# Performance work log

Measured on AMD Instinct MI355X. Metric: run time of the kernel, lower is better.

Reference implementation:

```python
import jax, jax.numpy as jnp
import numpy as np

B, S, C = 4096, 6, 2048  # batch, num_strips, in_channel
D = C // 8               # query/key projection dim

def setup_inputs() -> dict:
    key = jax.random.key(0)
    k1, k2, k3, k4 = jax.random.split(key, 4)
    sc = 1.0 / np.sqrt(C)
    return {
        "x": jax.random.normal(k1, (B, S, C), dtype=jnp.float32),
        "Wq": jax.random.normal(k2, (D, C), dtype=jnp.float32) * sc,
        "Wk": jax.random.normal(k3, (D, C), dtype=jnp.float32) * sc,
        "Wv": jax.random.normal(k4, (C, C), dtype=jnp.float32) * sc,
        "gamma": jnp.ones((1,), dtype=jnp.float32),
    }

def reference(x, Wq, Wk, Wv, gamma):
    # x: [B, S, C] stacked squeezed strips (feat in the torch code)
    q = jnp.einsum('bsc,dc->bsd', x, Wq)          # [B, S, D]
    k = jnp.einsum('bsc,dc->bsd', x, Wk)          # [B, S, D]
    energy = jnp.einsum('bsd,btd->bst', q, k)     # [B, S, S]
    attention = jax.nn.softmax(energy, axis=-1)   # softmax over keys
    v = jnp.einsum('bsc,dc->bsd', x, Wv)          # [B, S, C]
    out = jnp.einsum('bst,btc->bsc', attention, v)  # [B, S, C]
    out = gamma * out + x                         # gamma-scaled residual
    return out, attention
```

## Files before the change

### kernel.cpp

```cpp
#include <hip/hip_runtime.h>

typedef __attribute__((ext_vector_type(4))) float f32x4;
typedef __attribute__((ext_vector_type(8))) _Float16 f16x8;
typedef __attribute__((ext_vector_type(4))) unsigned short u16x4;
typedef __attribute__((ext_vector_type(8))) unsigned short u16x8;

#define NB 4096
#define NS 6
#define NC 2048
#define MTOT (NB * NS)

static __device__ __forceinline__ unsigned short f2h_bits(float f) {
  _Float16 h = (_Float16)f;
  unsigned short b;
  __builtin_memcpy(&b, &h, 2);
  return b;
}
static __device__ __forceinline__ float h2f(unsigned short b) {
  _Float16 h;
  __builtin_memcpy(&h, &b, 2);
  return (float)h;
}

#define NX4 12582912
#define NW4 262144
#define NV4 1048576
__global__ void prep_all(const float* __restrict__ x, const float* __restrict__ Wq,
                         const float* __restrict__ Wk, const float* __restrict__ Wv,
                         unsigned short* __restrict__ xh, unsigned short* __restrict__ wqk,
                         unsigned short* __restrict__ wvh) {
  long i = blockIdx.x * blockDim.x + threadIdx.x;
  const long stride = (long)gridDim.x * blockDim.x;
  for (; i < NX4 + NW4 + NV4; i += stride) {
    f32x4 v;
    unsigned short* dst;
    long di;
    if (i < NX4) {
      v = reinterpret_cast<const f32x4*>(x)[i];
      dst = xh; di = i;
    } else if (i < NX4 + NW4) {
      const long j = i - NX4;
      const int row = (int)(j >> 9);
      const int col4 = (int)(j & 511);
      const float* src = (row < 256) ? (Wq + (size_t)row * NC)
                                     : (Wk + (size_t)(row - 256) * NC);
      v = reinterpret_cast<const f32x4*>(src)[col4];
      dst = wqk; di = j;
    } else {
      const long j = i - NX4 - NW4;
      v = reinterpret_cast<const f32x4*>(Wv)[j];
      dst = wvh; di = j;
    }
    u16x4 o;
#pragma unroll
    for (int j = 0; j < 4; ++j) o[j] = f2h_bits(v[j]);
    reinterpret_cast<u16x4*>(dst)[di] = o;
  }
}


#define FENCE() asm volatile("" ::: "memory")
#define BAR() do { FENCE(); __builtin_amdgcn_s_barrier(); FENCE(); } while (0)
#define VM4BAR() do { FENCE(); asm volatile("s_waitcnt vmcnt(4)" ::: "memory"); \
                      __builtin_amdgcn_s_barrier(); FENCE(); } while (0)

__device__ __forceinline__ void stage_op(const unsigned short* g, int row0, int k0,
                                         char* ldsOp, int wid, int lane) {
  const int sl = lane ^ ((lane >> 4) & 1) ^ (((lane >> 5) & 1) << 1);
#pragma unroll
  for (int h = 0; h < 2; ++h)
#pragma unroll
    for (int i = 0; i < 2; ++i) {
      const int c = wid * 2 + i;
      const unsigned short* src =
          g + (size_t)(row0 + h * 128 + (c >> 1) * 16 + (sl >> 2)) * 2048 +
          (unsigned)(k0 + (c & 1) * 32 + (sl & 3) * 8);
      __builtin_amdgcn_global_load_lds(
          (__attribute__((address_space(1))) void*)src,
          (__attribute__((address_space(3))) void*)(ldsOp + h * 16384 + c * 1024),
          16, 0, 0);
    }
}

template <int N, bool EPI, bool NFAST>
__global__ void __launch_bounds__(512, 2)
gemm256(const unsigned short* __restrict__ A, const unsigned short* __restrict__ B,
        float* __restrict__ C, const unsigned short* __restrict__ resid,
        const float* __restrict__ gam) {
  constexpr int NT = 2048 / 64;
  constexpr int MT = MTOT / 256;
  constexpr int NXT = N / 256;
  constexpr int NWG = MT * NXT;
  constexpr int CPX = NWG / 8;
  __shared__ char lds[131072];

  const int bid = blockIdx.x;
  const int wg = (bid & 7) * CPX + (bid >> 3);
  const int bx = NFAST ? (wg % NXT) : (wg / MT);
  const int by = NFAST ? (wg / NXT) : (wg % MT);
  const int m0 = by * 256, n0 = bx * 256;

  const int t = threadIdx.x;
  const int lane = t & 63;
  const int wid = t >> 6;
  const int wr = wid >> 2, wc = wid & 3;
  const int laneOff = (lane & 15) * 64 + (lane >> 4) * 16;
  const int swzOff = laneOff ^ (((laneOff >> 9) & 1) << 5) ^ (((laneOff >> 8) & 1) << 4);
  const int aBase = wr * 16384 + swzOff;
  const int bBase = 32768 + (wc >> 1) * 16384 + (wc & 1) * 8192 + swzOff;

  f32x4 acc[8][4] = {};

#define WRAPT(TT) ((TT) >= NT ? (TT) - NT : (TT))
#define STAGE_A(TT) stage_op(A, m0, WRAPT(TT) * 64, lds + ((TT) & 1) * 65536, wid, lane)
#define STAGE_B(TT) stage_op(B, n0, WRAPT(TT) * 64, lds + ((TT) & 1) * 65536 + 32768, wid, lane)

  STAGE_A(0);
  STAGE_B(0);
  STAGE_B(1);
  VM4BAR();

  for (int tau = 0; tau < NT; ++tau) {
    char* bufc = lds + (tau & 1) * 65536;
    STAGE_A(tau + 1);
    f16x8 Af[8], Bf[4];
#pragma unroll
    for (int m = 0; m < 4; ++m) {
      Af[m]     = *reinterpret_cast<const f16x8*>(bufc + aBase + (m * 2) * 1024);
      Af[4 + m] = *reinterpret_cast<const f16x8*>(bufc + aBase + 8192 + (m * 2) * 1024);
    }
#pragma unroll
    for (int n = 0; n < 4; ++n)
      Bf[n] = *reinterpret_cast<const f16x8*>(bufc + bBase + (n * 2) * 1024);
    __builtin_amdgcn_s_setprio(1);
#pragma unroll
    for (int m = 0; m < 8; ++m)
#pragma unroll
      for (int n = 0; n < 4; ++n)
        acc[m][n] = __builtin_amdgcn_mfma_f32_16x16x32_f16(Af[m], Bf[n], acc[m][n], 0, 0, 0);
    __builtin_amdgcn_s_setprio(0);
    f16x8 Ag[8], Bg[4];
#pragma unroll
    for (int m = 0; m < 4; ++m) {
      Ag[m]     = *reinterpret_cast<const f16x8*>(bufc + aBase + (m * 2 + 1) * 1024);
      Ag[4 + m] = *reinterpret_cast<const f16x8*>(bufc + aBase + 8192 + (m * 2 + 1) * 1024);
    }
#pragma unroll
    for (int n = 0; n < 4; ++n)
      Bg[n] = *reinterpret_cast<const f16x8*>(bufc + bBase + (n * 2 + 1) * 1024);
    BAR();
    STAGE_B(tau + 2);
    VM4BAR();
    __builtin_amdgcn_s_setprio(1);
#pragma unroll
    for (int m = 0; m < 8; ++m)
#pragma unroll
      for (int n = 0; n < 4; ++n)
        acc[m][n] = __builtin_amdgcn_mfma_f32_16x16x32_f16(Ag[m], Bg[n], acc[m][n], 0, 0, 0);
    __builtin_amdgcn_s_setprio(0);
    BAR();
  }

#undef STAGE_A
#undef STAGE_B
#undef WRAPT

  const float g = EPI ? gam[0] : 0.f;
#pragma unroll
  for (int m = 0; m < 8; ++m)
#pragma unroll
    for (int n = 0; n < 4; ++n)
#pragma unroll
      for (int j = 0; j < 4; ++j) {
        const int r = m0 + wr * 128 + m * 16 + (lane >> 4) * 4 + j;
        const int c = n0 + wc * 64 + n * 16 + (lane & 15);
        const size_t idx = (size_t)r * (size_t)N + (size_t)c;
        float v = acc[m][n][j];
        if (EPI) v = g * v + h2f(resid[idx]);
        C[idx] = v;
      }
}

__global__ void __launch_bounds__(256)
attn_fuse(const float* __restrict__ QK,
          const unsigned short* __restrict__ xh,
          float* __restrict__ attn_out,
          unsigned short* __restrict__ y)
{
  __shared__ float qk[NS * 512];
  __shared__ float eng[36];
  __shared__ float att[36];
  const int b = blockIdx.x;
  const int t = threadIdx.x;
  {
    const f32x4* src = reinterpret_cast<const f32x4*>(QK + (size_t)b * (NS * 512));
    f32x4* dst = reinterpret_cast<f32x4*>(qk);
    for (int i = t; i < (NS * 512) / 4; i += 256) dst[i] = src[i];
  }
  __syncthreads();
  if (t < 144) {
    const int s = t / 24;
    const int rem = t - s * 24;
    const int u = rem >> 2;
    const int sub = rem & 3;
    const float* qr = qk + s * 512;
    const float* kr = qk + u * 512 + 256;
    float sum = 0.f;
    const int d0 = sub * 64;
#pragma unroll 4
    for (int d = 0; d < 64; ++d) sum += qr[d0 + d] * kr[d0 + d];
    sum += __shfl_xor(sum, 1);
    sum += __shfl_xor(sum, 2);
    if (sub == 0) eng[s * 6 + u] = sum;
  }
  __syncthreads();
  if (t < 6) {
    float e[6];
#pragma unroll
    for (int u = 0; u < 6; ++u) e[u] = eng[t * 6 + u];
    float mx = e[0];
#pragma unroll
    for (int u = 1; u < 6; ++u) mx = fmaxf(mx, e[u]);
    float p[6];
    float sm = 0.f;
#pragma unroll
    for (int u = 0; u < 6; ++u) { p[u] = expf(e[u] - mx); sm += p[u]; }
    const float inv = 1.0f / sm;
#pragma unroll
    for (int u = 0; u < 6; ++u) {
      const float a = p[u] * inv;
      att[t * 6 + u] = a;
      attn_out[(size_t)b * 36 + t * 6 + u] = a;
    }
  }
  __syncthreads();
  const unsigned short* xb = xh + (size_t)b * (NS * NC);
  unsigned short* yb = y + (size_t)b * (NS * NC);
  const int c0 = t * 8;
  f32x4 xv[12];
#pragma unroll
  for (int u = 0; u < 6; ++u) {
    u16x8 v = *reinterpret_cast<const u16x8*>(xb + u * NC + c0);
#pragma unroll
    for (int j = 0; j < 4; ++j) {
      xv[2 * u][j] = h2f(v[j]);
      xv[2 * u + 1][j] = h2f(v[4 + j]);
    }
  }
#pragma unroll
  for (int s = 0; s < 6; ++s) {
    f32x4 a0 = 0.f, a1 = 0.f;
#pragma unroll
    for (int u = 0; u < 6; ++u) {
      const float w = att[s * 6 + u];
      a0 += w * xv[2 * u];
      a1 += w * xv[2 * u + 1];
    }
    u16x8 o;
#pragma unroll
    for (int j = 0; j < 4; ++j) { o[j] = f2h_bits(a0[j]); o[4 + j] = f2h_bits(a1[j]); }
    *reinterpret_cast<u16x8*>(yb + s * NC + c0) = o;
  }
}

extern "C" void kernel_launch(void* const* d_in, const int* in_sizes, int n_in,
                              void* d_out, int out_size, void* d_ws, size_t ws_size,
                              hipStream_t stream) {
  (void)in_sizes; (void)n_in; (void)out_size; (void)ws_size;
  const float* x   = (const float*)d_in[0];
  const float* Wq  = (const float*)d_in[1];
  const float* Wk  = (const float*)d_in[2];
  const float* Wv  = (const float*)d_in[3];
  const float* gam = (const float*)d_in[4];
  float* out = (float*)d_out;
  float* attn_out = out + (size_t)MTOT * NC;

  char* ws = (char*)d_ws;
  unsigned short* xh  = (unsigned short*)(ws);
  unsigned short* yb  = (unsigned short*)(ws + 100663296ull);
  unsigned short* wqk = (unsigned short*)(ws + 201326592ull);
  unsigned short* wvh = (unsigned short*)(ws + 203423744ull);
  float*          qkb = (float*)(ws + 211812352ull);

  prep_all<<<2048, 256, 0, stream>>>(x, Wq, Wk, Wv, xh, wqk, wvh);

  gemm256<512, false, false><<<192, 512, 0, stream>>>(
      xh, wqk, qkb, nullptr, nullptr);

  attn_fuse<<<NB, 256, 0, stream>>>(qkb, xh, attn_out, yb);

  gemm256<2048, true, true><<<768, 512, 0, stream>>>(
      yb, wvh, out, xh, gam);
}
```

Baseline: 410.3 us.

## Restructure GEMM main loop into quadrant-wise LDS loads interleaved with half-tile staging

Splits each 256x256x64 iteration into four quadrant MFMA phases (M-half by N-half). Each phase is preceded by LDS fragment reads for only the needed quadrant and by a half-tile global-to-LDS stage. The aim is to interleave memory traffic with MFMA work at a finer grain and to cut live fragment registers. The cost is more barriers per iteration and explicit lgkmcnt waits, and the B buffer overwrite ordering now depends on these barriers.

New measurement: 402.9 us. About the same (-1.8%).

```diff
diff --git a/kernel.cpp b/kernel.cpp
--- a/kernel.cpp
+++ b/kernel.cpp
@@ -63,23 +63,22 @@
 #define BAR() do { FENCE(); __builtin_amdgcn_s_barrier(); FENCE(); } while (0)
 #define VM4BAR() do { FENCE(); asm volatile("s_waitcnt vmcnt(4)" ::: "memory"); \
                       __builtin_amdgcn_s_barrier(); FENCE(); } while (0)
-
-__device__ __forceinline__ void stage_op(const unsigned short* g, int row0, int k0,
-                                         char* ldsOp, int wid, int lane) {
+#define LGKM0() do { asm volatile("s_waitcnt lgkmcnt(0)" ::: "memory"); \
+                     __builtin_amdgcn_sched_barrier(0); } while (0)
+
+__device__ __forceinline__ void stage_half(const unsigned short* g, int row0, int k0,
+                                           char* region, int wid, int lane) {
   const int sl = lane ^ ((lane >> 4) & 1) ^ (((lane >> 5) & 1) << 1);
 #pragma unroll
-  for (int h = 0; h < 2; ++h)
-#pragma unroll
-    for (int i = 0; i < 2; ++i) {
-      const int c = wid * 2 + i;
-      const unsigned short* src =
-          g + (size_t)(row0 + h * 128 + (c >> 1) * 16 + (sl >> 2)) * 2048 +
-          (unsigned)(k0 + (c & 1) * 32 + (sl & 3) * 8);
-      __builtin_amdgcn_global_load_lds(
-          (__attribute__((address_space(1))) void*)src,
-          (__attribute__((address_space(3))) void*)(ldsOp + h * 16384 + c * 1024),
-          16, 0, 0);
-    }
+  for (int i = 0; i < 2; ++i) {
+    const int c = wid * 2 + i;
+    const unsigned short* src =
+        g + (size_t)(row0 + (c >> 1) * 16 + (sl >> 2)) * 2048 +
+        (unsigned)(k0 + (c & 1) * 32 + (sl & 3) * 8);
+    __builtin_amdgcn_global_load_lds(
+        (__attribute__((address_space(1))) void*)src,
+        (__attribute__((address_space(3))) void*)(region + c * 1024), 16, 0, 0);
+  }
 }
 
 template <int N, bool EPI, bool NFAST>
@@ -106,63 +105,63 @@
   const int wr = wid >> 2, wc = wid & 3;
   const int laneOff = (lane & 15) * 64 + (lane >> 4) * 16;
   const int swzOff = laneOff ^ (((laneOff >> 9) & 1) << 5) ^ (((laneOff >> 8) & 1) << 4);
-  const int aBase = wr * 16384 + swzOff;
-  const int bBase = 32768 + (wc >> 1) * 16384 + (wc & 1) * 8192 + swzOff;
 
   f32x4 acc[8][4] = {};
+  f16x8 Aq[4][2], B0q[2][2], B1q[2][2];
 
 #define WRAPT(TT) ((TT) >= NT ? (TT) - NT : (TT))
-#define STAGE_A(TT) stage_op(A, m0, WRAPT(TT) * 64, lds + ((TT) & 1) * 65536, wid, lane)
-#define STAGE_B(TT) stage_op(B, n0, WRAPT(TT) * 64, lds + ((TT) & 1) * 65536 + 32768, wid, lane)
-
-  STAGE_A(0);
-  STAGE_B(0);
-  STAGE_B(1);
+#define LDA(MH) do { _Pragma("unroll") for (int fm = 0; fm < 4; ++fm) \
+    _Pragma("unroll") for (int kk = 0; kk < 2; ++kk) \
+      Aq[fm][kk] = *reinterpret_cast<const f16x8*>( \
+          bufc + wr * 16384 + ((((MH) * 4 + fm) * 2 + kk)) * 1024 + swzOff); } while (0)
+#define LDB(NH, BQ) do { _Pragma("unroll") for (int fn = 0; fn < 2; ++fn) \
+    _Pragma("unroll") for (int kk = 0; kk < 2; ++kk) \
+      BQ[fn][kk] = *reinterpret_cast<const f16x8*>( \
+          bufc + 32768 + (wc >> 1) * 16384 + \
+          ((((wc & 1) * 4 + (NH) * 2 + fn) * 2 + kk)) * 1024 + swzOff); } while (0)
+#define MFQ(MH, NH, BQ) do { __builtin_amdgcn_s_setprio(1); \
+    _Pragma("unroll") for (int fm = 0; fm < 4; ++fm) \
+      _Pragma("unroll") for (int fn = 0; fn < 2; ++fn) \
+        _Pragma("unroll") for (int kk = 0; kk < 2; ++kk) \
+          acc[(MH) * 4 + fm][(NH) * 2 + fn] = __builtin_amdgcn_mfma_f32_16x16x32_f16( \
+              Aq[fm][kk], BQ[fn][kk], acc[(MH) * 4 + fm][(NH) * 2 + fn], 0, 0, 0); \
+    __builtin_amdgcn_s_setprio(0); } while (0)
+
+  stage_half(A, m0,       0,  lds,         wid, lane);
+  stage_half(A, m0 + 128, 0,  lds + 16384, wid, lane);
+  stage_half(B, n0,       0,  lds + 32768, wid, lane);
+  stage_half(B, n0 + 128, 0,  lds + 49152, wid, lane);
+  stage_half(B, n0,       64, lds + 65536 + 32768, wid, lane);
+  stage_half(B, n0 + 128, 64, lds + 65536 + 49152, wid, lane);
   VM4BAR();
 
   for (int tau = 0; tau < NT; ++tau) {
     char* bufc = lds + (tau & 1) * 65536;
-    STAGE_A(tau + 1);
-    f16x8 Af[8], Bf[4];
-#pragma unroll
-    for (int m = 0; m < 4; ++m) {
-      Af[m]     = *reinterpret_cast<const f16x8*>(bufc + aBase + (m * 2) * 1024);
-      Af[4 + m] = *reinterpret_cast<const f16x8*>(bufc + aBase + 8192 + (m * 2) * 1024);
-    }
-#pragma unroll
-    for (int n = 0; n < 4; ++n)
-      Bf[n] = *reinterpret_cast<const f16x8*>(bufc + bBase + (n * 2) * 1024);
-    __builtin_amdgcn_s_setprio(1);
-#pragma unroll
-    for (int m = 0; m < 8; ++m)
-#pragma unroll
-      for (int n = 0; n < 4; ++n)
-        acc[m][n] = __builtin_amdgcn_mfma_f32_16x16x32_f16(Af[m], Bf[n], acc[m][n], 0, 0, 0);
-    __builtin_amdgcn_s_setprio(0);
-    f16x8 Ag[8], Bg[4];
-#pragma unroll
-    for (int m = 0; m < 4; ++m) {
-      Ag[m]     = *reinterpret_cast<const f16x8*>(bufc + aBase + (m * 2 + 1) * 1024);
-      Ag[4 + m] = *reinterpret_cast<const f16x8*>(bufc + aBase + 8192 + (m * 2 + 1) * 1024);
-    }
-#pragma unroll
-    for (int n = 0; n < 4; ++n)
-      Bg[n] = *reinterpret_cast<const f16x8*>(bufc + bBase + (n * 2 + 1) * 1024);
+    char* bufo = lds + ((tau & 1) ^ 1) * 65536;
+    LDA(0);
+    LDB(0, B0q);
+    stage_half(A, m0, WRAPT(tau + 1) * 64, bufo, wid, lane);
     BAR();
-    STAGE_B(tau + 2);
+    LGKM0();
+    MFQ(0, 0, B0q);
+    LDB(1, B1q);
+    stage_half(A, m0 + 128, WRAPT(tau + 1) * 64, bufo + 16384, wid, lane);
+    BAR();
+    LGKM0();
+    MFQ(0, 1, B1q);
+    LDA(1);
+    stage_half(B, n0, WRAPT(tau + 2) * 64, bufc + 32768, wid, lane);
+    BAR();
+    LGKM0();
+    MFQ(1, 1, B1q);
+    stage_half(B, n0 + 128, WRAPT(tau + 2) * 64, bufc + 49152, wid, lane);
     VM4BAR();
-    __builtin_amdgcn_s_setprio(1);
-#pragma unroll
-    for (int m = 0; m < 8; ++m)
-#pragma unroll
-      for (int n = 0; n < 4; ++n)
-        acc[m][n] = __builtin_amdgcn_mfma_f32_16x16x32_f16(Ag[m], Bg[n], acc[m][n], 0, 0, 0);
-    __builtin_amdgcn_s_setprio(0);
-    BAR();
-  }
-
-#undef STAGE_A
-#undef STAGE_B
+    MFQ(1, 0, B0q);
+  }
+
+#undef MFQ
+#undef LDB
+#undef LDA
 #undef WRAPT
 
   const float g = EPI ? gam[0] : 0.f;
```
